# Performance work log

Hardware: AMD Instinct MI355X
Metric: run time of the kernel (lower is better)

The kernel has to match this reference:

```python
import jax, jax.numpy as jnp
import numpy as np

BAG = 15          # bag_size
STEPS = 5
LAM = 1e-3        # anti_hebb_lambda
PS = 8            # patch_size
IM = 28           # image_size
DEN = IM - PS     # position normalization denominator (=20)
KEEP = 0.1        # 1 - recurrent_sparsity


def _ln(h, gamma, beta, eps=1e-5):
    mu = jnp.mean(h, axis=-1, keepdims=True)
    var = jnp.mean((h - mu) ** 2, axis=-1, keepdims=True)
    return (h - mu) * jax.lax.rsqrt(var + eps) * gamma + beta


def _patch(img, pos):
    # img: [IM, IM], pos: [2] int32 -> flattened PSxPS patch [PS*PS]
    return jax.lax.dynamic_slice(img, (pos[0], pos[1]), (PS, PS)).reshape(PS * PS)

_extract = jax.vmap(_patch)  # [B,IM,IM], [B,2] -> [B, PS*PS]


def setup_inputs() -> dict:
    key = jax.random.key(0)
    ks = jax.random.split(key, 8)
    B = 65536
    x = jax.random.normal(ks[0], (B, 1, IM, IM), jnp.float32)
    in_dim = PS * PS + 2
    Wi = jax.random.normal(ks[1], (BAG, in_dim), jnp.float32) * np.sqrt(2.0 / in_dim)
    bi = jnp.zeros((BAG,), jnp.float32)
    gamma = jnp.ones((BAG,), jnp.float32)
    beta = jnp.zeros((BAG,), jnp.float32)
    mask = (jax.random.uniform(ks[2], (BAG, BAG)) < KEEP).astype(jnp.float32)
    R = jax.random.normal(ks[3], (BAG, BAG), jnp.float32) * np.sqrt(2.0 / BAG) * mask
    rb = jnp.zeros((BAG,), jnp.float32)
    Wc = jax.random.normal(ks[4], (2, BAG), jnp.float32) * np.sqrt(2.0 / BAG)
    bc = jnp.zeros((2,), jnp.float32)
    Wo = jax.random.normal(ks[5], (10, BAG), jnp.float32) * np.sqrt(2.0 / BAG)
    bo = jnp.zeros((10,), jnp.float32)
    return dict(x=x, Wi=Wi, bi=bi, gamma=gamma, beta=beta, R=R, rb=rb,
                mask=mask, Wc=Wc, bc=bc, Wo=Wo, bo=bo)


def reference(x, Wi, bi, gamma, beta, R, rb, mask, Wc, bc, Wo, bo):
    B = x.shape[0]
    imgs = x[:, 0]  # [B, IM, IM]
    positions = jnp.full((B, 2), (IM - PS) // 2, dtype=jnp.int32)
    state = None
    logits = None
    for _ in range(STEPS):  # small fixed step count; state/positions recur
        flat = _extract(imgs, positions)                       # [B, 64]
        pos = positions.astype(x.dtype) / DEN * 2.0 - 1.0      # [B, 2]
        in_act = jnp.concatenate([flat, pos], axis=1) @ Wi.T + bi
        if state is None:
            state = _ln(jax.nn.relu(in_act), gamma, beta)
        else:
            coact = jnp.einsum('bi,bj->ij', state, state) / B  # [BAG, BAG]
            Reff = (R - LAM * coact) * mask
            state = _ln(jax.nn.relu(in_act + state @ Reff.T + rb), gamma, beta)
        logits = state @ Wo.T + bo                             # [B, 10]
        ctrl = jnp.tanh(state @ Wc.T + bc)                     # [B, 2]
        mag_r = jnp.abs(ctrl[:, 0])
        mag_c = jnp.abs(ctrl[:, 1])
        row_sel = mag_r >= mag_c
        row_move = jnp.where(row_sel, jnp.sign(ctrl[:, 0]).astype(jnp.int32), 0)
        col_move = jnp.where(row_sel, 0, jnp.sign(ctrl[:, 1]).astype(jnp.int32))
        positions = jnp.clip(positions + jnp.stack([row_move, col_move], axis=1), 0, IM - PS)
    return logits
```

## Files before the change

kernel.cpp:

```cpp
#include <hip/hip_runtime.h>
#include <math.h>

#define IMSZ 28
#define PSZ  8
#define LAMF 0.001f
#define CSTRIDE 240
#define SSTR 17
#define MAXBLK 256

__global__ __launch_bounds__(1024, 4) void fused5(
    const float* __restrict__ x,
    const float* __restrict__ Wi, const float* __restrict__ bi,
    const float* __restrict__ gamma, const float* __restrict__ beta,
    const float* __restrict__ R, const float* __restrict__ rb,
    const float* __restrict__ mask,
    const float* __restrict__ Wc, const float* __restrict__ bc,
    const float* __restrict__ Wo, const float* __restrict__ bo,
    float* __restrict__ coact, unsigned* __restrict__ bar,
    float* __restrict__ out, float invB, int nblk)
{
    __shared__ float sWi[15 * 72];
    __shared__ float sBi[16], sGa[16], sBe[16], sRb[16];
    __shared__ float sWc[32], sBc[2], sWo[160], sBo[16];
    __shared__ float sRm[226], sLm[226];
    __shared__ float sReff[240];
    __shared__ float sCoQ[4][226];
    __shared__ float sS[256 * SSTR];

    const int tid = threadIdx.x;

    for (int idx = tid; idx < 990; idx += 1024) {
        int u = idx / 66, k = idx - u * 66;
        sWi[u * 72 + k] = Wi[idx];
    }
    if (tid < 15) {
        sBi[tid] = bi[tid]; sGa[tid] = gamma[tid];
        sBe[tid] = beta[tid]; sRb[tid] = rb[tid];
    }
    if (tid >= 32 && tid < 62)  sWc[tid - 32] = Wc[tid - 32];
    if (tid >= 62 && tid < 64)  sBc[tid - 62] = bc[tid - 62];
    if (tid >= 96 && tid < 246) sWo[tid - 96] = Wo[tid - 96];
    if (tid >= 246 && tid < 256) sBo[tid - 246] = bo[tid - 246];
    if (tid >= 256 && tid < 481) {
        int t = tid - 256;
        float m = mask[t];
        sRm[t] = R[t] * m;
        sLm[t] = (LAMF * invB) * m;
    }
    if (tid >= 481 && tid < 496) sReff[tid - 256] = 0.0f;
    __syncthreads();

    const int g = tid >> 3;
    const int c = tid & 7;
    const int b0 = blockIdx.x * 256 + g;
    const int b1 = b0 + 128;
    const float* img0 = x + (size_t)b0 * (IMSZ * IMSZ);
    const float* img1 = x + (size_t)b1 * (IMSZ * IMSZ);

    int pr0 = 10, pc0 = 10, pr1 = 10, pc1 = 10;
    float hA[15], hB[15];

    for (int s = 0; s < 5; ++s) {
        float sj0A = 0.f, sj1A = 0.f, sj0B = 0.f, sj1B = 0.f;
        if (s > 0) {
            sj0A = sS[g * SSTR + c];
            sj0B = sS[(g + 128) * SSTR + c];
            if (c < 7) {
                sj1A = sS[g * SSTR + 8 + c];
                sj1B = sS[(g + 128) * SSTR + 8 + c];
            }
            {
                const int q = tid >> 8;
                const int t = tid & 255;
                if (t < 225) {
                    const float* cb = coact
                        + ((size_t)(s - 1) * MAXBLK + q * 64) * CSTRIDE + t;
                    float a0 = 0.f, a1 = 0.f, a2 = 0.f, a3 = 0.f;
#pragma unroll 4
                    for (int k = 0; k < 64; k += 4) {
                        a0 += __hip_atomic_load(cb + (size_t)(k + 0) * CSTRIDE,
                                __ATOMIC_RELAXED, __HIP_MEMORY_SCOPE_AGENT);
                        a1 += __hip_atomic_load(cb + (size_t)(k + 1) * CSTRIDE,
                                __ATOMIC_RELAXED, __HIP_MEMORY_SCOPE_AGENT);
                        a2 += __hip_atomic_load(cb + (size_t)(k + 2) * CSTRIDE,
                                __ATOMIC_RELAXED, __HIP_MEMORY_SCOPE_AGENT);
                        a3 += __hip_atomic_load(cb + (size_t)(k + 3) * CSTRIDE,
                                __ATOMIC_RELAXED, __HIP_MEMORY_SCOPE_AGENT);
                    }
                    sCoQ[q][t] = (a0 + a1) + (a2 + a3);
                }
            }
            __syncthreads();
            if (tid < 225) {
                float cv = (sCoQ[0][tid] + sCoQ[1][tid])
                         + (sCoQ[2][tid] + sCoQ[3][tid]);
                sReff[tid] = sRm[tid] - sLm[tid] * cv;
            }
            __syncthreads();
        }

        float pA[8], pB[8];
        {
            const float* q0 = img0 + pr0 * IMSZ + pc0 + c;
            const float* q1 = img1 + pr1 * IMSZ + pc1 + c;
#pragma unroll
            for (int r = 0; r < 8; ++r) { pA[r] = q0[r * IMSZ]; pB[r] = q1[r * IMSZ]; }
        }

        const float fr0 = ((float)pr0 / 20.0f) * 2.0f - 1.0f;
        const float fc0 = ((float)pc0 / 20.0f) * 2.0f - 1.0f;
        const float fr1 = ((float)pr1 / 20.0f) * 2.0f - 1.0f;
        const float fc1 = ((float)pc1 / 20.0f) * 2.0f - 1.0f;

#pragma unroll
        for (int u = 0; u < 15; ++u) {
            float a = 0.f, bq = 0.f;
            const float* w = sWi + u * 72 + c;
#pragma unroll
            for (int r = 0; r < 8; ++r) {
                float wv = w[r * 8];
                a  = fmaf(pA[r], wv, a);
                bq = fmaf(pB[r], wv, bq);
            }
            if (s > 0) {
                float w0 = sReff[u * 15 + c];
                float w1 = sReff[u * 15 + 8 + c];
                a  = fmaf(sj0A, w0, a);  a  = fmaf(sj1A, w1, a);
                bq = fmaf(sj0B, w0, bq); bq = fmaf(sj1B, w1, bq);
            }
            if (c == 0) {
                float wr = sWi[u * 72 + 64], wc = sWi[u * 72 + 65];
                float bias = sBi[u] + ((s > 0) ? sRb[u] : 0.0f);
                a  = fmaf(fr0, wr, a);  a  = fmaf(fc0, wc, a);  a  += bias;
                bq = fmaf(fr1, wr, bq); bq = fmaf(fc1, wc, bq); bq += bias;
            }
            hA[u] = a; hB[u] = bq;
        }

#pragma unroll
        for (int u = 0; u < 15; ++u) {
            float vA = hA[u], vB = hB[u];
            vA += __shfl_xor(vA, 1); vB += __shfl_xor(vB, 1);
            vA += __shfl_xor(vA, 2); vB += __shfl_xor(vB, 2);
            vA += __shfl_xor(vA, 4); vB += __shfl_xor(vB, 4);
            hA[u] = fmaxf(vA, 0.0f);
            hB[u] = fmaxf(vB, 0.0f);
        }

        float muA = 0.f, muB = 0.f;
#pragma unroll
        for (int u = 0; u < 15; ++u) { muA += hA[u]; muB += hB[u]; }
        muA *= (1.0f / 15.0f); muB *= (1.0f / 15.0f);
        float vA = 0.f, vB = 0.f;
#pragma unroll
        for (int u = 0; u < 15; ++u) {
            float dA = hA[u] - muA; vA = fmaf(dA, dA, vA);
            float dB = hB[u] - muB; vB = fmaf(dB, dB, vB);
        }
        vA *= (1.0f / 15.0f); vB *= (1.0f / 15.0f);
        const float rsA = 1.0f / sqrtf(vA + 1e-5f);
        const float rsB = 1.0f / sqrtf(vB + 1e-5f);
#pragma unroll
        for (int u = 0; u < 15; ++u) {
            hA[u] = (hA[u] - muA) * rsA * sGa[u] + sBe[u];
            hB[u] = (hB[u] - muB) * rsB * sGa[u] + sBe[u];
        }

        if (s == 4) {
#pragma unroll
            for (int rep = 0; rep < 2; ++rep) {
                int o = rep * 8 + c;
                if (o < 10) {
                    float a0 = 0.f, a1 = 0.f;
#pragma unroll
                    for (int j = 0; j < 15; ++j) {
                        a0 = fmaf(hA[j], sWo[o * 15 + j], a0);
                        a1 = fmaf(hB[j], sWo[o * 15 + j], a1);
                    }
                    out[(size_t)b0 * 10 + o] = a0 + sBo[o];
                    out[(size_t)b1 * 10 + o] = a1 + sBo[o];
                }
            }
        } else {
            float c0A = 0.f, c1A = 0.f, c0B = 0.f, c1B = 0.f;
#pragma unroll
            for (int j = 0; j < 15; ++j) {
                c0A = fmaf(hA[j], sWc[j],      c0A);
                c1A = fmaf(hA[j], sWc[15 + j], c1A);
                c0B = fmaf(hB[j], sWc[j],      c0B);
                c1B = fmaf(hB[j], sWc[15 + j], c1B);
            }
            c0A = tanhf(c0A + sBc[0]); c1A = tanhf(c1A + sBc[1]);
            c0B = tanhf(c0B + sBc[0]); c1B = tanhf(c1B + sBc[1]);
            {
                float m0 = fabsf(c0A), m1 = fabsf(c1A);
                int rm, cm;
                if (m0 >= m1) { rm = (c0A > 0.f) - (c0A < 0.f); cm = 0; }
                else          { rm = 0; cm = (c1A > 0.f) - (c1A < 0.f); }
                pr0 = min(max(pr0 + rm, 0), IMSZ - PSZ);
                pc0 = min(max(pc0 + cm, 0), IMSZ - PSZ);
            }
            {
                float m0 = fabsf(c0B), m1 = fabsf(c1B);
                int rm, cm;
                if (m0 >= m1) { rm = (c0B > 0.f) - (c0B < 0.f); cm = 0; }
                else          { rm = 0; cm = (c1B > 0.f) - (c1B < 0.f); }
                pr1 = min(max(pr1 + rm, 0), IMSZ - PSZ);
                pc1 = min(max(pc1 + cm, 0), IMSZ - PSZ);
            }

#pragma unroll
            for (int k = 0; k < 8; ++k) {
                if (c == k) {
                    sS[g * SSTR + k]         = hA[k];
                    sS[(g + 128) * SSTR + k] = hB[k];
                    if (k < 7) {
                        sS[g * SSTR + 8 + k]         = hA[8 + k];
                        sS[(g + 128) * SSTR + 8 + k] = hB[8 + k];
                    }
                }
            }
            __syncthreads();

            {
                const int q = tid >> 8;
                const int t = tid & 255;
                if (t < 225) {
                    int i = t / 15, j = t - i * 15;
                    const int base = q * 64;
                    float a0 = 0.f, a1 = 0.f, a2 = 0.f, a3 = 0.f;
#pragma unroll
                    for (int bb = 0; bb < 64; bb += 4) {
                        a0 = fmaf(sS[(base + bb + 0) * SSTR + i], sS[(base + bb + 0) * SSTR + j], a0);
                        a1 = fmaf(sS[(base + bb + 1) * SSTR + i], sS[(base + bb + 1) * SSTR + j], a1);
                        a2 = fmaf(sS[(base + bb + 2) * SSTR + i], sS[(base + bb + 2) * SSTR + j], a2);
                        a3 = fmaf(sS[(base + bb + 3) * SSTR + i], sS[(base + bb + 3) * SSTR + j], a3);
                    }
                    sCoQ[q][t] = (a0 + a1) + (a2 + a3);
                }
            }
            __syncthreads();

            if (tid < 225) {
                float v = (sCoQ[0][tid] + sCoQ[1][tid])
                        + (sCoQ[2][tid] + sCoQ[3][tid]);
                __hip_atomic_store(
                    &coact[((size_t)s * MAXBLK + blockIdx.x) * CSTRIDE + tid], v,
                    __ATOMIC_RELAXED, __HIP_MEMORY_SCOPE_AGENT);
            }
            __syncthreads();

            if (tid == 0)
                __hip_atomic_store(&bar[s * MAXBLK + blockIdx.x], 1u,
                                   __ATOMIC_RELAXED, __HIP_MEMORY_SCOPE_AGENT);
            if (tid < 64) {
                const unsigned* bs = bar + s * MAXBLK;
                for (;;) {
                    unsigned f = 1u;
#pragma unroll
                    for (int k = 0; k < 4; ++k) {
                        int b = tid + k * 64;
                        unsigned v = (b < nblk)
                            ? __hip_atomic_load(&bs[b], __ATOMIC_RELAXED,
                                                __HIP_MEMORY_SCOPE_AGENT)
                            : 1u;
                        f &= v;
                    }
                    if (__all(f != 0)) break;
                    __builtin_amdgcn_s_sleep(1);
                }
            }
            __syncthreads();
        }
    }
}

extern "C" void kernel_launch(void* const* d_in, const int* in_sizes, int n_in,
                              void* d_out, int out_size, void* d_ws, size_t ws_size,
                              hipStream_t stream) {
    (void)n_in; (void)out_size; (void)ws_size;
    const float* x     = (const float*)d_in[0];
    const float* Wi    = (const float*)d_in[1];
    const float* bi    = (const float*)d_in[2];
    const float* gamma = (const float*)d_in[3];
    const float* beta  = (const float*)d_in[4];
    const float* R     = (const float*)d_in[5];
    const float* rb    = (const float*)d_in[6];
    const float* mask  = (const float*)d_in[7];
    const float* Wc    = (const float*)d_in[8];
    const float* bc    = (const float*)d_in[9];
    const float* Wo    = (const float*)d_in[10];
    const float* bo    = (const float*)d_in[11];
    float* out = (float*)d_out;

    const int B = in_sizes[0] / (IMSZ * IMSZ);
    const float invB = 1.0f / (float)B;
    int grid = B / 256;

    unsigned* bar = (unsigned*)d_ws;
    float* coact = (float*)((char*)d_ws + 4 * MAXBLK * sizeof(unsigned));

    hipMemsetAsync(d_ws, 0, (size_t)4 * MAXBLK * sizeof(unsigned), stream);

    fused5<<<grid, 1024, 0, stream>>>(
        x, Wi, bi, gamma, beta, R, rb, mask, Wc, bc, Wo, bo,
        coact, bar, out, invB, grid);
}
```

Before: 396.5 us.

## Replace all-to-all grid barrier with master-block reduction and broadcast flag

After: 404.8 us. 2.1% more time.

```diff
diff --git a/kernel.cpp b/kernel.cpp
--- a/kernel.cpp
+++ b/kernel.cpp
@@ -16,7 +16,8 @@
     const float* __restrict__ mask,
     const float* __restrict__ Wc, const float* __restrict__ bc,
     const float* __restrict__ Wo, const float* __restrict__ bo,
-    float* __restrict__ coact, unsigned* __restrict__ bar,
+    float* __restrict__ slots, float* __restrict__ cvbuf,
+    unsigned* __restrict__ bar, unsigned* __restrict__ ready,
     float* __restrict__ out, float invB, int nblk)
 {
     __shared__ float sWi[15 * 72];
@@ -69,34 +70,76 @@
                 sj1A = sS[g * SSTR + 8 + c];
                 sj1B = sS[(g + 128) * SSTR + 8 + c];
             }
-            {
-                const int q = tid >> 8;
-                const int t = tid & 255;
-                if (t < 225) {
-                    const float* cb = coact
-                        + ((size_t)(s - 1) * MAXBLK + q * 64) * CSTRIDE + t;
-                    float a0 = 0.f, a1 = 0.f, a2 = 0.f, a3 = 0.f;
+
+            if (blockIdx.x == 0) {
+                if (tid < 64) {
+                    const unsigned* bs = bar + (s - 1) * MAXBLK;
+                    for (;;) {
+                        unsigned f = 1u;
+#pragma unroll
+                        for (int k = 0; k < 4; ++k) {
+                            int b = tid + k * 64;
+                            unsigned v = (b < nblk)
+                                ? __hip_atomic_load(&bs[b], __ATOMIC_RELAXED,
+                                                    __HIP_MEMORY_SCOPE_AGENT)
+                                : 1u;
+                            f &= v;
+                        }
+                        if (__all(f != 0)) break;
+                        __builtin_amdgcn_s_sleep(2);
+                    }
+                }
+                __syncthreads();
+                {
+                    const int q = tid >> 8;
+                    const int t = tid & 255;
+                    if (t < 225) {
+                        const float* cb = slots
+                            + ((size_t)(s - 1) * MAXBLK + q * 64) * CSTRIDE + t;
+                        float a0 = 0.f, a1 = 0.f, a2 = 0.f, a3 = 0.f;
 #pragma unroll 4
-                    for (int k = 0; k < 64; k += 4) {
-                        a0 += __hip_atomic_load(cb + (size_t)(k + 0) * CSTRIDE,
-                                __ATOMIC_RELAXED, __HIP_MEMORY_SCOPE_AGENT);
-                        a1 += __hip_atomic_load(cb + (size_t)(k + 1) * CSTRIDE,
-                                __ATOMIC_RELAXED, __HIP_MEMORY_SCOPE_AGENT);
-                        a2 += __hip_atomic_load(cb + (size_t)(k + 2) * CSTRIDE,
-                                __ATOMIC_RELAXED, __HIP_MEMORY_SCOPE_AGENT);
-                        a3 += __hip_atomic_load(cb + (size_t)(k + 3) * CSTRIDE,
-                                __ATOMIC_RELAXED, __HIP_MEMORY_SCOPE_AGENT);
-                    }
-                    sCoQ[q][t] = (a0 + a1) + (a2 + a3);
-                }
-            }
-            __syncthreads();
-            if (tid < 225) {
-                float cv = (sCoQ[0][tid] + sCoQ[1][tid])
-                         + (sCoQ[2][tid] + sCoQ[3][tid]);
-                sReff[tid] = sRm[tid] - sLm[tid] * cv;
-            }
-            __syncthreads();
+                        for (int k = 0; k < 64; k += 4) {
+                            int sb = q * 64 + k;
+                            a0 += (sb + 0 < nblk) ? __hip_atomic_load(cb + (size_t)(k + 0) * CSTRIDE,
+                                    __ATOMIC_RELAXED, __HIP_MEMORY_SCOPE_AGENT) : 0.f;
+                            a1 += (sb + 1 < nblk) ? __hip_atomic_load(cb + (size_t)(k + 1) * CSTRIDE,
+                                    __ATOMIC_RELAXED, __HIP_MEMORY_SCOPE_AGENT) : 0.f;
+                            a2 += (sb + 2 < nblk) ? __hip_atomic_load(cb + (size_t)(k + 2) * CSTRIDE,
+                                    __ATOMIC_RELAXED, __HIP_MEMORY_SCOPE_AGENT) : 0.f;
+                            a3 += (sb + 3 < nblk) ? __hip_atomic_load(cb + (size_t)(k + 3) * CSTRIDE,
+                                    __ATOMIC_RELAXED, __HIP_MEMORY_SCOPE_AGENT) : 0.f;
+                        }
+                        sCoQ[q][t] = (a0 + a1) + (a2 + a3);
+                    }
+                }
+                __syncthreads();
+                if (tid < 225) {
+                    float cv = (sCoQ[0][tid] + sCoQ[1][tid])
+                             + (sCoQ[2][tid] + sCoQ[3][tid]);
+                    __hip_atomic_store(&cvbuf[(s - 1) * CSTRIDE + tid], cv,
+                                       __ATOMIC_RELAXED, __HIP_MEMORY_SCOPE_AGENT);
+                    sReff[tid] = sRm[tid] - sLm[tid] * cv;
+                }
+                __syncthreads();
+                if (tid == 0)
+                    __hip_atomic_store(&ready[(s - 1) * 16], 1u,
+                                       __ATOMIC_RELAXED, __HIP_MEMORY_SCOPE_AGENT);
+            } else {
+                if (tid < 64) {
+                    while (__hip_atomic_load(&ready[(s - 1) * 16],
+                                             __ATOMIC_RELAXED,
+                                             __HIP_MEMORY_SCOPE_AGENT) == 0u)
+                        __builtin_amdgcn_s_sleep(8);
+                }
+                __syncthreads();
+                if (tid < 225) {
+                    float cv = __hip_atomic_load(&cvbuf[(s - 1) * CSTRIDE + tid],
+                                                 __ATOMIC_RELAXED,
+                                                 __HIP_MEMORY_SCOPE_AGENT);
+                    sReff[tid] = sRm[tid] - sLm[tid] * cv;
+                }
+                __syncthreads();
+            }
         }
 
         float pA[8], pB[8];
@@ -245,7 +288,7 @@
                 float v = (sCoQ[0][tid] + sCoQ[1][tid])
                         + (sCoQ[2][tid] + sCoQ[3][tid]);
                 __hip_atomic_store(
-                    &coact[((size_t)s * MAXBLK + blockIdx.x) * CSTRIDE + tid], v,
+                    &slots[((size_t)s * MAXBLK + blockIdx.x) * CSTRIDE + tid], v,
                     __ATOMIC_RELAXED, __HIP_MEMORY_SCOPE_AGENT);
             }
             __syncthreads();
@@ -253,24 +296,6 @@
             if (tid == 0)
                 __hip_atomic_store(&bar[s * MAXBLK + blockIdx.x], 1u,
                                    __ATOMIC_RELAXED, __HIP_MEMORY_SCOPE_AGENT);
-            if (tid < 64) {
-                const unsigned* bs = bar + s * MAXBLK;
-                for (;;) {
-                    unsigned f = 1u;
-#pragma unroll
-                    for (int k = 0; k < 4; ++k) {
-                        int b = tid + k * 64;
-                        unsigned v = (b < nblk)
-                            ? __hip_atomic_load(&bs[b], __ATOMIC_RELAXED,
-                                                __HIP_MEMORY_SCOPE_AGENT)
-                            : 1u;
-                        f &= v;
-                    }
-                    if (__all(f != 0)) break;
-                    __builtin_amdgcn_s_sleep(1);
-                }
-            }
-            __syncthreads();
         }
     }
 }
@@ -297,12 +322,14 @@
     const float invB = 1.0f / (float)B;
     int grid = B / 256;
 
-    unsigned* bar = (unsigned*)d_ws;
-    float* coact = (float*)((char*)d_ws + 4 * MAXBLK * sizeof(unsigned));
-
-    hipMemsetAsync(d_ws, 0, (size_t)4 * MAXBLK * sizeof(unsigned), stream);
+    unsigned* bar   = (unsigned*)d_ws;
+    unsigned* ready = bar + 4 * MAXBLK;
+    float* cvbuf    = (float*)(ready + 4 * 16);
+    float* slots    = cvbuf + 4 * CSTRIDE;
+
+    hipMemsetAsync(d_ws, 0, (size_t)(4 * MAXBLK + 4 * 16) * sizeof(unsigned), stream);
 
     fused5<<<grid, 1024, 0, stream>>>(
         x, Wi, bi, gamma, beta, R, rb, mask, Wc, bc, Wo, bo,
-        coact, bar, out, invB, grid);
+        slots, cvbuf, bar, ready, out, invB, grid);
 }
```
